# Performance work log

Hardware: AMD Instinct MI355X
Metric: run time of the kernel (lower is better)

## Reference

```python
import jax, jax.numpy as jnp
import numpy as np

K_NEIGHBORS = 16
N_CLASSES = 10


def setup_inputs() -> dict:
    key = jax.random.key(0)
    k1, k2, k3 = jax.random.split(key, 3)
    x = jax.random.normal(k1, (2048, 128), dtype=jnp.float32)
    train_data = jax.random.normal(k2, (100000, 128), dtype=jnp.float32)
    train_labels = jax.random.randint(k3, (100000,), 0, N_CLASSES, dtype=jnp.int64)
    return {"x": x, "train_data": train_data, "train_labels": train_labels}


def reference(x, train_data, train_labels):
    N = x.shape[0]
    x2 = jnp.sum(x * x, axis=1, keepdims=True)            # [N, 1]
    t2 = jnp.sum(train_data * train_data, axis=1)          # [M]
    d2 = x2 + t2[None, :] - 2.0 * (x @ train_data.T)       # [N, M]
    dist = jnp.sqrt(jnp.maximum(d2, 0.0))
    # smallest-k via top_k on negated distances
    neg_d, idx = jax.lax.top_k(-dist, K_NEIGHBORS)         # [N, K]
    d = -neg_d
    labels = train_labels[idx]                              # [N, K]
    # weights == 'distance': inverse distance; rows containing an exact match
    # (inf weight) get a 0/1 indicator vector instead.
    w = 1.0 / d
    inf_mask = jnp.isinf(w)
    inf_row = jnp.any(inf_mask, axis=1, keepdims=True)
    w = jnp.where(inf_row, inf_mask.astype(jnp.float32), w)
    # weighted vote: scatter-add weights into per-class buckets
    rows = jnp.arange(N)[:, None]
    proba = jnp.zeros((N, N_CLASSES), jnp.float32).at[rows, labels].add(w)
    s = jnp.sum(proba, axis=1, keepdims=True)
    s = jnp.where(s == 0.0, 1.0, s)
    proba = proba / s
    pred = jnp.argmax(proba, axis=1)
    return pred, proba
```

## Files before the change

### kernel.cpp

```cpp
#include <hip/hip_runtime.h>
#include <hip/hip_fp16.h>
#include <math.h>

#define M_TRAIN 100000
#define NQ 2048
#define DIM 128
#define KNN 16
#define NCLS 10

#define S_STRIDE 16
#define S_CNT (M_TRAIN / S_STRIDE)
#define S_PAD 6272
#define SCH 49
#define SPC 128
#define TT 64
#define MQ 128
#define QSTR 136

#define CAP 768
#define TBH 50176
#define NTR 128
#define NQT 64
#define MARGIN 3.0f

using bfrag = __attribute__((ext_vector_type(8))) short;
using cfrag = __attribute__((ext_vector_type(4))) float;

__device__ __forceinline__ bool better(float d1, int i1, float d2, int i2) {
    return (d1 < d2) || (d1 == d2 && i1 < i2);
}

__device__ __forceinline__ unsigned pack_bf16(float a, float b) {
    unsigned ua = __float_as_uint(a), ub = __float_as_uint(b);
    ua += 0x7fffu + ((ua >> 16) & 1u);
    ub += 0x7fffu + ((ub >> 16) & 1u);
    return (ua >> 16) | (ub & 0xffff0000u);
}

__device__ __forceinline__ bfrag pack_bf16x8(const float* p) {
    union { unsigned u[4]; bfrag f; } r;
    r.u[0] = pack_bf16(p[0], p[1]);
    r.u[1] = pack_bf16(p[2], p[3]);
    r.u[2] = pack_bf16(p[4], p[5]);
    r.u[3] = pack_bf16(p[6], p[7]);
    return r.f;
}

__device__ __forceinline__ void gload_lds16(const void* g, void* l) {
    __builtin_amdgcn_global_load_lds(
        (const __attribute__((address_space(1))) unsigned int*)g,
        (__attribute__((address_space(3))) unsigned int*)l, 16, 0, 0);
}

__global__ void knn_norms(const float* __restrict__ train,
                          const float* __restrict__ x,
                          float* __restrict__ t2, float* __restrict__ x2) {
    int gw = (blockIdx.x * blockDim.x + threadIdx.x) >> 6;
    int lane = threadIdx.x & 63;
    if (gw >= M_TRAIN + NQ) return;
    const float* r = (gw < M_TRAIN) ? (train + (size_t)gw * DIM)
                                    : (x + (size_t)(gw - M_TRAIN) * DIM);
    float a = r[lane];
    float b = r[lane + 64];
    float s = a * a + b * b;
    #pragma unroll
    for (int off = 32; off > 0; off >>= 1)
        s += __shfl_down(s, off, 64);
    if (lane == 0) {
        if (gw < M_TRAIN) t2[gw] = s; else x2[gw - M_TRAIN] = s;
    }
}

__global__ void knn_zero_cnt(int* __restrict__ cnt) {
    int i = blockIdx.x * blockDim.x + threadIdx.x;
    if (i < NQ) cnt[i] = 0;
}

__global__ __launch_bounds__(256, 2)
void knn_sub_mfma(const float* __restrict__ x, const float* __restrict__ train,
                  const float* __restrict__ t2, const float* __restrict__ x2,
                  __half* __restrict__ dsub) {
    __shared__ short Q[MQ * QSTR];
    __shared__ short T[TT * QSTR];
    __shared__ float t2h[TT];
    int tid = threadIdx.x;
    int w = tid >> 6, lane = tid & 63;
    int rquad = lane >> 4, rcol = lane & 15;
    int qBase = blockIdx.y * MQ;
    int cBase = blockIdx.x * SPC;

    #pragma unroll
    for (int it = 0; it < 16; ++it) {
        int f = it * 256 + tid;
        int row = f >> 5, c4 = f & 31;
        float4 v = ((const float4*)x)[(size_t)(qBase + row) * (DIM / 4) + c4];
        uint2 p; p.x = pack_bf16(v.x, v.y); p.y = pack_bf16(v.z, v.w);
        *(uint2*)&Q[row * QSTR + c4 * 4] = p;
    }
    __syncthreads();

    float x2r[2][4];
    #pragma unroll
    for (int rt = 0; rt < 2; ++rt)
        #pragma unroll
        for (int reg = 0; reg < 4; ++reg)
            x2r[rt][reg] = x2[qBase + w * 32 + rt * 16 + rquad * 4 + reg];

    bfrag A[2][4];
    #pragma unroll
    for (int rt = 0; rt < 2; ++rt)
        #pragma unroll
        for (int ks = 0; ks < 4; ++ks) {
            int r = w * 32 + rt * 16 + rcol;
            A[rt][ks] = *(const bfrag*)&Q[r * QSTR + ks * 32 + rquad * 8];
        }

    const cfrag zero4 = {0.f, 0.f, 0.f, 0.f};
    for (int t = 0; t < 2; ++t) {
        __syncthreads();
        int sBase = cBase + t * TT;
        #pragma unroll
        for (int it = 0; it < 8; ++it) {
            int f = it * 256 + tid;
            int row = f >> 5, c4 = f & 31;
            int sj = sBase + row;
            bool ok = sj < S_CNT;
            float4 v = ok ? ((const float4*)train)[(size_t)sj * S_STRIDE * (DIM / 4) + c4]
                          : make_float4(0.f, 0.f, 0.f, 0.f);
            uint2 p; p.x = pack_bf16(v.x, v.y); p.y = pack_bf16(v.z, v.w);
            *(uint2*)&T[row * QSTR + c4 * 4] = p;
        }
        if (tid < TT) {
            int sj = sBase + tid;
            t2h[tid] = (sj < S_CNT) ? t2[(size_t)sj * S_STRIDE] : 1e30f;
        }
        __syncthreads();

        cfrag acc[2][4];
        #pragma unroll
        for (int ks = 0; ks < 4; ++ks) {
            bfrag B[4];
            #pragma unroll
            for (int ct = 0; ct < 4; ++ct) {
                int n = ct * 16 + rcol;
                B[ct] = *(const bfrag*)&T[n * QSTR + ks * 32 + rquad * 8];
            }
            #pragma unroll
            for (int rt = 0; rt < 2; ++rt)
                #pragma unroll
                for (int ct = 0; ct < 4; ++ct)
                    acc[rt][ct] = (ks == 0)
                        ? __builtin_amdgcn_mfma_f32_16x16x32_bf16(A[rt][0], B[ct], zero4, 0, 0, 0)
                        : __builtin_amdgcn_mfma_f32_16x16x32_bf16(A[rt][ks], B[ct], acc[rt][ct], 0, 0, 0);
        }

        float th[4];
        #pragma unroll
        for (int ct = 0; ct < 4; ++ct) th[ct] = t2h[ct * 16 + rcol];
        #pragma unroll
        for (int rt = 0; rt < 2; ++rt)
            #pragma unroll
            for (int ct = 0; ct < 4; ++ct)
                #pragma unroll
                for (int reg = 0; reg < 4; ++reg) {
                    float d2 = x2r[rt][reg] + th[ct] - 2.f * acc[rt][ct][reg];
                    int qrow = qBase + w * 32 + rt * 16 + rquad * 4 + reg;
                    int col = sBase + ct * 16 + rcol;
                    dsub[(size_t)qrow * S_PAD + col] = __float2half_rn(d2);
                }
    }
}

__global__ __launch_bounds__(256)
void knn_select(const __half* __restrict__ dsub, float* __restrict__ tau) {
    __shared__ float wv[4];
    __shared__ int   wc[4];
    __shared__ float sv;
    __shared__ int   sc;
    int q = blockIdx.x, tid = threadIdx.x;
    int w = tid >> 6, lane = tid & 63;

    float bd[KNN];
    #pragma unroll
    for (int j = 0; j < KNN; ++j) bd[j] = 3.4e38f;
    for (int k = 0; k < 25; ++k) {
        int idx = k * 256 + tid;
        if (idx < S_PAD) {
            float v = __half2float(dsub[(size_t)q * S_PAD + idx]);
            if (v < bd[KNN - 1]) {
                bd[KNN - 1] = v;
                #pragma unroll
                for (int j = KNN - 1; j >= 1; --j)
                    if (bd[j] < bd[j - 1]) { float t = bd[j]; bd[j] = bd[j - 1]; bd[j - 1] = t; }
            }
        }
    }

    float last = 3.4e38f;
    for (int sel = 0; sel < KNN; ++sel) {
        float mv = bd[0]; int mj = 0;
        #pragma unroll
        for (int j = 1; j < KNN; ++j) if (bd[j] < mv) { mv = bd[j]; mj = j; }
        int mc = (tid << 4) | mj;
        #pragma unroll
        for (int off = 32; off > 0; off >>= 1) {
            float ov = __shfl_down(mv, off, 64);
            int   oc = __shfl_down(mc, off, 64);
            if (ov < mv) { mv = ov; mc = oc; }
        }
        if (lane == 0) { wv[w] = mv; wc[w] = mc; }
        __syncthreads();
        if (tid == 0) {
            float bv = wv[0]; int bc = wc[0];
            #pragma unroll
            for (int i = 1; i < 4; ++i) if (wv[i] < bv) { bv = wv[i]; bc = wc[i]; }
            sv = bv; sc = bc;
        }
        __syncthreads();
        last = sv;
        if (tid == (sc >> 4)) {
            int j0 = sc & 15;
            #pragma unroll
            for (int j = 0; j < KNN; ++j) if (j == j0) bd[j] = 3.4e38f;
        }
        __syncthreads();
    }
    if (tid == 0) tau[q] = last;
}

__global__ __launch_bounds__(256)
void knn_convert_bf16(const float* __restrict__ train,
                      unsigned int* __restrict__ tb, int rowBase) {
    int i = blockIdx.x * 256 + threadIdx.x;
    int row = i >> 5, seg = i & 31;
    int g = rowBase + row;
    float4 v = (g < M_TRAIN)
        ? ((const float4*)train)[(size_t)g * (DIM / 4) + seg]
        : make_float4(0.f, 0.f, 0.f, 0.f);
    uint2 p; p.x = pack_bf16(v.x, v.y); p.y = pack_bf16(v.z, v.w);
    int off = (seg * 8) ^ ((row & 7) << 4);
    *(uint2*)((char*)tb + (size_t)row * 256 + off) = p;
}

__global__ __launch_bounds__(256, 4)
void knn_filter4(const float* __restrict__ x, const short* __restrict__ tbb,
                 const float* __restrict__ t2, const float* __restrict__ x2,
                 const float* __restrict__ tau, int pBase0,
                 int* __restrict__ buf_i, int* __restrict__ cnt) {
    __shared__ __align__(16) short T[NTR * DIM];
    int tid = threadIdx.x;
    int w = tid >> 6, lane = tid & 63;
    int rquad = lane >> 4, rcol = lane & 15;

    int bid = blockIdx.x;
    int xcd = bid & 7, r = bid >> 3;
    int qb = r & 31;
    int nch = xcd + 8 * (r >> 5);
    int qBase = qb * NQT;
    int tbase = pBase0 + nch * NTR;

    const char* gsrc = (const char*)tbb + (size_t)nch * NTR * 256 + w * 8192 + lane * 16;
    char* ldst = (char*)T + w * 8192;
    #pragma unroll
    for (int i = 0; i < 8; ++i)
        gload_lds16(gsrc + i * 1024, ldst + i * 1024);

    bfrag A[4];
    int qrow = qBase + w * 16 + rcol;
    #pragma unroll
    for (int ks = 0; ks < 4; ++ks)
        A[ks] = pack_bf16x8(&x[(size_t)qrow * DIM + ks * 32 + rquad * 8]);

    float RC[4];
    #pragma unroll
    for (int reg = 0; reg < 4; ++reg) {
        int q = qBase + w * 16 + rquad * 4 + reg;
        RC[reg] = 0.5f * (x2[q] - tau[q] - MARGIN);
    }
    float th[8];
    #pragma unroll
    for (int ct = 0; ct < 8; ++ct)
        th[ct] = 0.5f * t2[tbase + ct * 16 + rcol];
    __syncthreads();

    int swz = (rcol & 7) << 4;
    int cs[4];
    #pragma unroll
    for (int ks = 0; ks < 4; ++ks)
        cs[ks] = (ks * 64 + rquad * 16) ^ swz;

    const cfrag zero4 = {0.f, 0.f, 0.f, 0.f};
    cfrag acc[8];
    #pragma unroll
    for (int ks = 0; ks < 4; ++ks)
        #pragma unroll
        for (int ct = 0; ct < 8; ++ct) {
            const bfrag B = *(const bfrag*)((const char*)T + (ct * 16 + rcol) * 256 + cs[ks]);
            acc[ct] = (ks == 0)
                ? __builtin_amdgcn_mfma_f32_16x16x32_bf16(A[0], B, zero4, 0, 0, 0)
                : __builtin_amdgcn_mfma_f32_16x16x32_bf16(A[ks], B, acc[ct], 0, 0, 0);
        }

    unsigned gm[4][8];
    int tot[4];
    #pragma unroll
    for (int reg = 0; reg < 4; ++reg) {
        int t = 0;
        #pragma unroll
        for (int ct = 0; ct < 8; ++ct) {
            int idx = tbase + ct * 16 + rcol;
            bool pass = (acc[ct][reg] >= RC[reg] + th[ct]) && (idx < M_TRAIN);
            unsigned long long m = __ballot(pass);
            unsigned g = (unsigned)(m >> (rquad * 16)) & 0xFFFFu;
            gm[reg][ct] = g;
            t += __popc(g);
        }
        tot[reg] = t;
    }
    int baseR[4];
    #pragma unroll
    for (int reg = 0; reg < 4; ++reg) {
        int q = qBase + w * 16 + rquad * 4 + reg;
        if (rcol == 0) baseR[reg] = atomicAdd(&cnt[q], tot[reg]);
    }
    int lsrc = lane & 48;
    unsigned lb = 1u << rcol;
    #pragma unroll
    for (int reg = 0; reg < 4; ++reg) {
        int q = qBase + w * 16 + rquad * 4 + reg;
        int b = __shfl(baseR[reg], lsrc, 64);
        int off = 0;
        #pragma unroll
        for (int ct = 0; ct < 8; ++ct) {
            unsigned g = gm[reg][ct];
            if (g & lb) {
                int slot = b + off + __popc(g & (lb - 1));
                if (slot < CAP)
                    buf_i[(size_t)q * CAP + slot] = tbase + ct * 16 + rcol;
            }
            off += __popc(g);
        }
    }
}

__global__ __launch_bounds__(256)
void knn_final(const float* __restrict__ x,
               const float* __restrict__ train,
               const float* __restrict__ t2v,
               const float* __restrict__ x2v,
               const int* __restrict__ buf_i,
               const int* __restrict__ cnt,
               const int* __restrict__ labels,
               float* __restrict__ out) {
    __shared__ float sd[CAP];
    __shared__ int   si[CAP];
    __shared__ float spr[NCLS];
    int q = blockIdx.x;
    int tid = threadIdx.x;
    int w = tid >> 6, lane = tid & 63;
    int grp = lane >> 4;
    int sub = lane & 15;
    int n = cnt[q]; if (n > CAP) n = CAP;

    const float4* xq = (const float4*)&x[(size_t)q * DIM + sub * 8];
    float4 qa = xq[0], qb = xq[1];
    float x2l = x2v[q];

    for (int base = 0; base < n; base += 16) {
        int i = base + w * 4 + grp;
        if (i < n) {
            int idx = buf_i[(size_t)q * CAP + i];
            const float4* tr = (const float4*)&train[(size_t)idx * DIM + sub * 8];
            float4 ta = tr[0], tb4 = tr[1];
            float s = qa.x * ta.x + qa.y * ta.y + qa.z * ta.z + qa.w * ta.w
                    + qb.x * tb4.x + qb.y * tb4.y + qb.z * tb4.z + qb.w * tb4.w;
            s += __shfl_xor(s, 1, 64);
            s += __shfl_xor(s, 2, 64);
            s += __shfl_xor(s, 4, 64);
            s += __shfl_xor(s, 8, 64);
            if (sub == 0) { sd[i] = x2l + t2v[idx] - 2.f * s; si[i] = idx; }
        }
    }
    __syncthreads();

    float kd[KNN];
    int   ki[KNN];
    for (int sel = 0; sel < KNN; ++sel) {
        if (w == 0) {
            float md = 3.4e38f; int mi = 0x7fffffff; int ml = -1;
            for (int i = lane; i < n; i += 64)
                if (better(sd[i], si[i], md, mi)) { md = sd[i]; mi = si[i]; ml = i; }
            #pragma unroll
            for (int off = 32; off > 0; off >>= 1) {
                float od = __shfl_down(md, off, 64);
                int   oi = __shfl_down(mi, off, 64);
                int   ol = __shfl_down(ml, off, 64);
                if (better(od, oi, md, mi)) { md = od; mi = oi; ml = ol; }
            }
            md = __shfl(md, 0, 64); mi = __shfl(mi, 0, 64); ml = __shfl(ml, 0, 64);
            kd[sel] = md; ki[sel] = mi;
            if (lane == 0 && ml >= 0) { sd[ml] = 3.4e38f; si[ml] = 0x7fffffff; }
        }
        __syncthreads();
    }

    if (tid == 0) {
        bool anyzero = false;
        float dist[KNN];
        #pragma unroll
        for (int j = 0; j < KNN; ++j) {
            dist[j] = sqrtf(fmaxf(kd[j], 0.f));
            if (dist[j] == 0.f) anyzero = true;
        }
        #pragma unroll
        for (int c = 0; c < NCLS; ++c) spr[c] = 0.f;
        #pragma unroll
        for (int j = 0; j < KNN; ++j) {
            int idxj = ki[j];
            if (idxj < 0 || idxj >= M_TRAIN) continue;
            float wgt = anyzero ? (dist[j] == 0.f ? 1.f : 0.f) : 1.f / dist[j];
            spr[labels[idxj]] += wgt;
        }
        float s = 0.f;
        #pragma unroll
        for (int c = 0; c < NCLS; ++c) s += spr[c];
        if (s == 0.f) s = 1.f;
        float inv = 1.f / s;
        float best = -1.f; int bc = 0;
        #pragma unroll
        for (int c = 0; c < NCLS; ++c) {
            float pv = spr[c] * inv;
            out[NQ + (size_t)q * NCLS + c] = pv;
            if (pv > best) { best = pv; bc = c; }
        }
        out[q] = (float)bc;
    }
}

extern "C" void kernel_launch(void* const* d_in, const int* in_sizes, int n_in,
                              void* d_out, int out_size, void* d_ws, size_t ws_size,
                              hipStream_t stream) {
    const float* x      = (const float*)d_in[0];
    const float* train  = (const float*)d_in[1];
    const int*   labels = (const int*)d_in[2];
    float* out = (float*)d_out;

    char* base = (char*)d_ws;
    float*  t2   = (float*)(base);
    float*  x2   = (float*)(base + 401408);
    float*  tau  = (float*)(base + 409600);
    int*    cnt  = (int*)  (base + 417792);
    char*   region = base + 425984;
    __half* dsub = (__half*)region;
    unsigned int* tb = (unsigned int*)region;
    int*    bi   = (int*)(region + 12845056);

    int nrows = M_TRAIN + NQ;
    knn_norms<<<(nrows * 64 + 255) / 256, 256, 0, stream>>>(train, x, t2, x2);
    knn_zero_cnt<<<(NQ + 255) / 256, 256, 0, stream>>>(cnt);

    dim3 gs(SCH, NQ / MQ);
    knn_sub_mfma<<<gs, 256, 0, stream>>>(x, train, t2, x2, dsub);

    knn_select<<<NQ, 256, 0, stream>>>(dsub, tau);

    for (int h = 0; h < 2; ++h) {
        int rowBase = h * TBH;
        knn_convert_bf16<<<(TBH * 32) / 256, 256, 0, stream>>>(train, tb, rowBase);
        knn_filter4<<<(TBH / NTR) * (NQ / NQT), 256, 0, stream>>>(
            x, (const short*)tb, t2, x2, tau, rowBase, bi, cnt);
    }

    knn_final<<<NQ, 256, 0, stream>>>(x, train, t2, x2, bi, cnt, labels, out);
}
```

Baseline: 412.4 us.

## Pre-convert queries to bf16 once and keep final top-k candidates in registers

```diff
diff --git a/kernel.cpp b/kernel.cpp
--- a/kernel.cpp
+++ b/kernel.cpp
@@ -35,15 +35,6 @@
     ua += 0x7fffu + ((ua >> 16) & 1u);
     ub += 0x7fffu + ((ub >> 16) & 1u);
     return (ua >> 16) | (ub & 0xffff0000u);
-}
-
-__device__ __forceinline__ bfrag pack_bf16x8(const float* p) {
-    union { unsigned u[4]; bfrag f; } r;
-    r.u[0] = pack_bf16(p[0], p[1]);
-    r.u[1] = pack_bf16(p[2], p[3]);
-    r.u[2] = pack_bf16(p[4], p[5]);
-    r.u[3] = pack_bf16(p[6], p[7]);
-    return r.f;
 }
 
 __device__ __forceinline__ void gload_lds16(const void* g, void* l) {
@@ -230,8 +221,19 @@
 
 __global__ __launch_bounds__(256)
 void knn_convert_bf16(const float* __restrict__ train,
-                      unsigned int* __restrict__ tb, int rowBase) {
-    int i = blockIdx.x * 256 + threadIdx.x;
+                      unsigned int* __restrict__ tb, int rowBase,
+                      const float* __restrict__ x,
+                      unsigned int* __restrict__ xb) {
+    int b = blockIdx.x;
+    if (b >= (TBH * 32) / 256) {
+        int i = (b - (TBH * 32) / 256) * 256 + threadIdx.x;
+        int row = i >> 5, seg = i & 31;
+        float4 v = ((const float4*)x)[(size_t)row * (DIM / 4) + seg];
+        uint2 p; p.x = pack_bf16(v.x, v.y); p.y = pack_bf16(v.z, v.w);
+        ((uint2*)xb)[(size_t)row * 32 + seg] = p;
+        return;
+    }
+    int i = b * 256 + threadIdx.x;
     int row = i >> 5, seg = i & 31;
     int g = rowBase + row;
     float4 v = (g < M_TRAIN)
@@ -243,7 +245,8 @@
 }
 
 __global__ __launch_bounds__(256, 4)
-void knn_filter4(const float* __restrict__ x, const short* __restrict__ tbb,
+void knn_filter5(const unsigned int* __restrict__ xbb,
+                 const short* __restrict__ tbb,
                  const float* __restrict__ t2, const float* __restrict__ x2,
                  const float* __restrict__ tau, int pBase0,
                  int* __restrict__ buf_i, int* __restrict__ cnt) {
@@ -267,9 +270,10 @@
 
     bfrag A[4];
     int qrow = qBase + w * 16 + rcol;
+    const char* xrow = (const char*)xbb + (size_t)qrow * 256;
     #pragma unroll
     for (int ks = 0; ks < 4; ++ks)
-        A[ks] = pack_bf16x8(&x[(size_t)qrow * DIM + ks * 32 + rquad * 8]);
+        A[ks] = *(const bfrag*)(xrow + ks * 64 + rquad * 16);
 
     float RC[4];
     #pragma unroll
@@ -354,7 +358,6 @@
                float* __restrict__ out) {
     __shared__ float sd[CAP];
     __shared__ int   si[CAP];
-    __shared__ float spr[NCLS];
     int q = blockIdx.x;
     int tid = threadIdx.x;
     int w = tid >> 6, lane = tid & 63;
@@ -383,57 +386,69 @@
     }
     __syncthreads();
 
-    float kd[KNN];
-    int   ki[KNN];
-    for (int sel = 0; sel < KNN; ++sel) {
-        if (w == 0) {
-            float md = 3.4e38f; int mi = 0x7fffffff; int ml = -1;
-            for (int i = lane; i < n; i += 64)
-                if (better(sd[i], si[i], md, mi)) { md = sd[i]; mi = si[i]; ml = i; }
+    if (w == 0) {
+        float bd[12]; int bi2[12];
+        #pragma unroll
+        for (int j = 0; j < 12; ++j) {
+            int i = lane + j * 64;
+            if (i < n) { bd[j] = sd[i]; bi2[j] = si[i]; }
+            else       { bd[j] = 3.4e38f; bi2[j] = 0x7fffffff; }
+        }
+        float kd[KNN]; int ki[KNN];
+        for (int sel = 0; sel < KNN; ++sel) {
+            float md = bd[0]; int mi = bi2[0]; int mc = (lane << 4);
+            #pragma unroll
+            for (int j = 1; j < 12; ++j)
+                if (better(bd[j], bi2[j], md, mi)) { md = bd[j]; mi = bi2[j]; mc = (lane << 4) | j; }
             #pragma unroll
             for (int off = 32; off > 0; off >>= 1) {
                 float od = __shfl_down(md, off, 64);
                 int   oi = __shfl_down(mi, off, 64);
-                int   ol = __shfl_down(ml, off, 64);
-                if (better(od, oi, md, mi)) { md = od; mi = oi; ml = ol; }
-            }
-            md = __shfl(md, 0, 64); mi = __shfl(mi, 0, 64); ml = __shfl(ml, 0, 64);
+                int   oc = __shfl_down(mc, off, 64);
+                if (better(od, oi, md, mi)) { md = od; mi = oi; mc = oc; }
+            }
+            md = __shfl(md, 0, 64); mi = __shfl(mi, 0, 64); mc = __shfl(mc, 0, 64);
             kd[sel] = md; ki[sel] = mi;
-            if (lane == 0 && ml >= 0) { sd[ml] = 3.4e38f; si[ml] = 0x7fffffff; }
-        }
-        __syncthreads();
-    }
-
-    if (tid == 0) {
-        bool anyzero = false;
-        float dist[KNN];
-        #pragma unroll
-        for (int j = 0; j < KNN; ++j) {
-            dist[j] = sqrtf(fmaxf(kd[j], 0.f));
-            if (dist[j] == 0.f) anyzero = true;
-        }
-        #pragma unroll
-        for (int c = 0; c < NCLS; ++c) spr[c] = 0.f;
-        #pragma unroll
-        for (int j = 0; j < KNN; ++j) {
-            int idxj = ki[j];
-            if (idxj < 0 || idxj >= M_TRAIN) continue;
-            float wgt = anyzero ? (dist[j] == 0.f ? 1.f : 0.f) : 1.f / dist[j];
-            spr[labels[idxj]] += wgt;
-        }
-        float s = 0.f;
-        #pragma unroll
-        for (int c = 0; c < NCLS; ++c) s += spr[c];
-        if (s == 0.f) s = 1.f;
-        float inv = 1.f / s;
-        float best = -1.f; int bc = 0;
-        #pragma unroll
-        for (int c = 0; c < NCLS; ++c) {
-            float pv = spr[c] * inv;
-            out[NQ + (size_t)q * NCLS + c] = pv;
-            if (pv > best) { best = pv; bc = c; }
-        }
-        out[q] = (float)bc;
+            if (lane == (mc >> 4)) {
+                int j0 = mc & 15;
+                #pragma unroll
+                for (int j = 0; j < 12; ++j)
+                    if (j == j0) { bd[j] = 3.4e38f; bi2[j] = 0x7fffffff; }
+            }
+        }
+
+        if (lane == 0) {
+            bool anyzero = false;
+            float dist[KNN];
+            #pragma unroll
+            for (int j = 0; j < KNN; ++j) {
+                dist[j] = sqrtf(fmaxf(kd[j], 0.f));
+                if (dist[j] == 0.f) anyzero = true;
+            }
+            float spr[NCLS];
+            #pragma unroll
+            for (int c = 0; c < NCLS; ++c) spr[c] = 0.f;
+            #pragma unroll
+            for (int j = 0; j < KNN; ++j) {
+                int idxj = ki[j];
+                if (idxj < 0 || idxj >= M_TRAIN) continue;
+                float wgt = anyzero ? (dist[j] == 0.f ? 1.f : 0.f) : 1.f / dist[j];
+                spr[labels[idxj]] += wgt;
+            }
+            float s = 0.f;
+            #pragma unroll
+            for (int c = 0; c < NCLS; ++c) s += spr[c];
+            if (s == 0.f) s = 1.f;
+            float inv = 1.f / s;
+            float best = -1.f; int bc = 0;
+            #pragma unroll
+            for (int c = 0; c < NCLS; ++c) {
+                float pv = spr[c] * inv;
+                out[NQ + (size_t)q * NCLS + c] = pv;
+                if (pv > best) { best = pv; bc = c; }
+            }
+            out[q] = (float)bc;
+        }
     }
 }
 
@@ -454,6 +469,7 @@
     __half* dsub = (__half*)region;
     unsigned int* tb = (unsigned int*)region;
     int*    bi   = (int*)(region + 12845056);
+    unsigned int* xb = (unsigned int*)(region + 19136512);
 
     int nrows = M_TRAIN + NQ;
     knn_norms<<<(nrows * 64 + 255) / 256, 256, 0, stream>>>(train, x, t2, x2);
@@ -466,9 +482,10 @@
 
     for (int h = 0; h < 2; ++h) {
         int rowBase = h * TBH;
-        knn_convert_bf16<<<(TBH * 32) / 256, 256, 0, stream>>>(train, tb, rowBase);
-        knn_filter4<<<(TBH / NTR) * (NQ / NQT), 256, 0, stream>>>(
-            x, (const short*)tb, t2, x2, tau, rowBase, bi, cnt);
+        int cgrid = (TBH * 32) / 256 + (h == 0 ? (NQ * 32) / 256 : 0);
+        knn_convert_bf16<<<cgrid, 256, 0, stream>>>(train, tb, rowBase, x, xb);
+        knn_filter5<<<(TBH / NTR) * (NQ / NQT), 256, 0, stream>>>(
+            xb, (const short*)tb, t2, x2, tau, rowBase, bi, cnt);
     }
 
     knn_final<<<NQ, 256, 0, stream>>>(x, train, t2, x2, bi, cnt, labels, out);
```

Result: faster. 401.0 us (-2.8%).
